# Performance work log

Hardware: AMD Instinct MI355X
Metric: run time of the kernel (lower is better)

Reference implementation:

```python
import jax, jax.numpy as jnp
import numpy as np

B = 16384
F_CONT = 128   # continuous features (Gaussian scopes)
F_CAT = 128    # integer-valued features (Categorical scopes)
NG = 1024      # number of Gaussian leaves
NC = 1024      # number of Categorical leaves
K = 32         # categorical classes
LOG_2PI = float(np.log(2.0 * np.pi))


def setup_inputs() -> dict:
    key = jax.random.key(0)
    k1, k2, k3, k4, k5, k6, k7 = jax.random.split(key, 7)
    # data: first F_CONT columns continuous, last F_CAT columns hold integer category values
    x_cont = jax.random.normal(k1, (B, F_CONT), dtype=jnp.float32)
    x_cat = jax.random.randint(k2, (B, F_CAT), 0, K).astype(jnp.float32)
    x = jnp.concatenate([x_cont, x_cat], axis=1)  # [B, 256]
    gauss_mean = jax.random.normal(k3, (NG,), dtype=jnp.float32)
    gauss_std = jax.random.uniform(k4, (NG,), dtype=jnp.float32, minval=0.5, maxval=2.0)
    cat_logp = jax.nn.log_softmax(jax.random.normal(k5, (NC, K), dtype=jnp.float32), axis=-1)
    gauss_scopes = jax.random.randint(k6, (NG,), 0, F_CONT)            # index into continuous cols
    cat_scopes = jax.random.randint(k7, (NC,), 0, F_CAT) + F_CONT      # index into categorical cols
    return {
        "x": x,
        "gauss_mean": gauss_mean,
        "gauss_std": gauss_std,
        "cat_logp": cat_logp,
        "gauss_scopes": gauss_scopes,
        "cat_scopes": cat_scopes,
    }


def reference(x, gauss_mean, gauss_std, cat_logp, gauss_scopes, cat_scopes):
    # Fused equivalent of the per-leaf Python loop: one gather + one formula per family.
    # Gaussian leaves: Normal(mean, std).log_prob(x[:, scope])
    gv = x[:, gauss_scopes]                                   # [B, NG]
    z = (gv - gauss_mean[None, :]) / gauss_std[None, :]
    g_ll = -0.5 * (z * z) - jnp.log(gauss_std)[None, :] - 0.5 * LOG_2PI
    # Categorical leaves: log p_i[x[:, scope_i]]
    cidx = x[:, cat_scopes].astype(jnp.int32)                 # [B, NC]
    c_ll = cat_logp[jnp.arange(cat_logp.shape[0])[None, :], cidx]  # [B, NC]
    return jnp.concatenate([g_ll, c_ll], axis=1)              # [B, NG+NC]
```

## Files before the change

kernel.cpp:

```cpp
#include <hip/hip_runtime.h>
#include <math.h>


#define HALF_LOG_2PI 0.91893853320467274178f

constexpr int BROWS   = 16384;
constexpr int FX      = 256;
constexpr int NG      = 1024;
constexpr int NC      = 1024;
constexpr int KCAT    = 32;
constexpr int OUTW    = NG + NC;
constexpr int ROWS_PB = 16;
constexpr int NTHR    = 256;
constexpr int XPITCH  = FX + 1;
constexpr int CCH     = 128;
constexpr int NCHUNK  = NC / CCH;
constexpr int CPITCH  = CCH + 4;

__global__ __launch_bounds__(NTHR) void leaves_kernel(
    const float* __restrict__ x,
    const float* __restrict__ gmean,
    const float* __restrict__ gstd,
    const float* __restrict__ clogp,
    const int*   __restrict__ gsc,
    const int*   __restrict__ csc,
    float*       __restrict__ out)
{
    __shared__ float xs[ROWS_PB * XPITCH];
    __shared__ float cts[ROWS_PB * CPITCH];

    const int t = threadIdx.x;
    const long long b0 = (long long)blockIdx.x * ROWS_PB;

    {
        const int r  = t >> 4;
        const int c0 = (t & 15) * 16;
        const float* src = x + (b0 + r) * FX + c0;
        float*       dst = xs + r * XPITCH + c0;
        #pragma unroll
        for (int q = 0; q < 4; ++q) {
            float4 v = ((const float4*)src)[q];
            dst[q * 4 + 0] = v.x; dst[q * 4 + 1] = v.y;
            dst[q * 4 + 2] = v.z; dst[q * 4 + 3] = v.w;
        }
    }

    const int4   g4 = ((const int4*)gsc)[t];
    const float4 mu = ((const float4*)gmean)[t];
    const float4 sd = ((const float4*)gstd)[t];
    float4 is, cc;
    is.x = 1.0f / sd.x;  cc.x = -logf(sd.x) - HALF_LOG_2PI;
    is.y = 1.0f / sd.y;  cc.y = -logf(sd.y) - HALF_LOG_2PI;
    is.z = 1.0f / sd.z;  cc.z = -logf(sd.z) - HALF_LOG_2PI;
    is.w = 1.0f / sd.w;  cc.w = -logf(sd.w) - HALF_LOG_2PI;

    __syncthreads();

    #pragma unroll
    for (int r = 0; r < ROWS_PB; ++r) {
        const float* xr = xs + r * XPITCH;
        float4 gres;
        { float z = (xr[g4.x] - mu.x) * is.x; gres.x = fmaf(-0.5f * z, z, cc.x); }
        { float z = (xr[g4.y] - mu.y) * is.y; gres.y = fmaf(-0.5f * z, z, cc.y); }
        { float z = (xr[g4.z] - mu.z) * is.z; gres.z = fmaf(-0.5f * z, z, cc.z); }
        { float z = (xr[g4.w] - mu.w) * is.w; gres.w = fmaf(-0.5f * z, z, cc.w); }
        ((float4*)(out + (b0 + r) * OUTW))[t] = gres;
    }

    const int w   = t >> 6;
    const int l   = t & 63;
    const int row = l & 15;
    const int co  = l >> 4;
    const float* xrp = xs + row * XPITCH;

    const int wr = t >> 4;
    const int wo = (t & 15) * 4;

    for (int chunk = 0; chunk < NCHUNK; ++chunk) {
        const int cb = chunk * CCH + w * 32 + co;

        int sc[8];
        #pragma unroll
        for (int j = 0; j < 8; ++j) sc[j] = csc[cb + j * 4];

        int ix[8];
        #pragma unroll
        for (int j = 0; j < 8; ++j) ix[j] = (int)xrp[sc[j]];

        float v[8];
        #pragma unroll
        for (int j = 0; j < 8; ++j) v[j] = clogp[(cb + j * 4) * KCAT + ix[j]];

        #pragma unroll
        for (int j = 0; j < 8; ++j)
            cts[row * CPITCH + w * 32 + j * 4 + co] = v[j];

        __syncthreads();

        {
            float4 a = *(const float4*)(cts + wr * CPITCH + wo);
            float4 b = *(const float4*)(cts + wr * CPITCH + wo + 64);
            float* dst = out + (b0 + wr) * OUTW + NG + chunk * CCH;
            *(float4*)(dst + wo)      = a;
            *(float4*)(dst + wo + 64) = b;
        }
        __syncthreads();
    }
}

extern "C" void kernel_launch(void* const* d_in, const int* in_sizes, int n_in,
                              void* d_out, int out_size, void* d_ws, size_t ws_size,
                              hipStream_t stream) {
    const float* x     = (const float*)d_in[0];
    const float* gmean = (const float*)d_in[1];
    const float* gstd  = (const float*)d_in[2];
    const float* clogp = (const float*)d_in[3];
    const int*   gsc   = (const int*)d_in[4];
    const int*   csc   = (const int*)d_in[5];
    float*       out   = (float*)d_out;

    leaves_kernel<<<dim3(BROWS / ROWS_PB), dim3(NTHR), 0, stream>>>(
        x, gmean, gstd, clogp, gsc, csc, out);
}
```

Measured before the change: 30.53 us.

## Double-buffer categorical staging tile and prefetch first chunk before Gaussian pass

The categorical staging buffer in shared memory is split into two halves. Each chunk's gathers now overlap with writing out the previous chunk, which removes one of the two barriers per chunk. The first chunk's dependent gathers (scope, x value, log-prob) are issued before the Gaussian output loop, so their latency hides behind the Gaussian stores. This costs extra shared memory and keeps eight values live across the Gaussian loop, which raises register pressure.

```diff
diff --git a/kernel.cpp b/kernel.cpp
--- a/kernel.cpp
+++ b/kernel.cpp
@@ -27,7 +27,7 @@
     float*       __restrict__ out)
 {
     __shared__ float xs[ROWS_PB * XPITCH];
-    __shared__ float cts[ROWS_PB * CPITCH];
+    __shared__ float cts[2][ROWS_PB * CPITCH];
 
     const int t = threadIdx.x;
     const long long b0 = (long long)blockIdx.x * ROWS_PB;
@@ -56,6 +56,25 @@
 
     __syncthreads();
 
+    const int w   = t >> 6;
+    const int l   = t & 63;
+    const int row = l & 15;
+    const int co  = l >> 4;
+    const float* xrp = xs + row * XPITCH;
+
+    const int wr = t >> 4;
+    const int wo = (t & 15) * 4;
+
+    float v[8];
+    {
+        const int cb = 0 * CCH + w * 32 + co;
+        #pragma unroll
+        for (int j = 0; j < 8; ++j) {
+            const int c = cb + j * 4;
+            v[j] = clogp[c * KCAT + (int)xrp[csc[c]]];
+        }
+    }
+
     #pragma unroll
     for (int r = 0; r < ROWS_PB; ++r) {
         const float* xr = xs + r * XPITCH;
@@ -67,44 +86,44 @@
         ((float4*)(out + (b0 + r) * OUTW))[t] = gres;
     }
 
-    const int w   = t >> 6;
-    const int l   = t & 63;
-    const int row = l & 15;
-    const int co  = l >> 4;
-    const float* xrp = xs + row * XPITCH;
+    #pragma unroll
+    for (int j = 0; j < 8; ++j)
+        cts[0][row * CPITCH + w * 32 + j * 4 + co] = v[j];
+    __syncthreads();
 
-    const int wr = t >> 4;
-    const int wo = (t & 15) * 4;
-
-    for (int chunk = 0; chunk < NCHUNK; ++chunk) {
+    for (int chunk = 1; chunk < NCHUNK; ++chunk) {
+        const int p  = chunk & 1;
         const int cb = chunk * CCH + w * 32 + co;
 
-        int sc[8];
         #pragma unroll
-        for (int j = 0; j < 8; ++j) sc[j] = csc[cb + j * 4];
+        for (int j = 0; j < 8; ++j) {
+            const int c = cb + j * 4;
+            v[j] = clogp[c * KCAT + (int)xrp[csc[c]]];
+        }
 
-        int ix[8];
-        #pragma unroll
-        for (int j = 0; j < 8; ++j) ix[j] = (int)xrp[sc[j]];
-
-        float v[8];
-        #pragma unroll
-        for (int j = 0; j < 8; ++j) v[j] = clogp[(cb + j * 4) * KCAT + ix[j]];
+        {
+            const float* src = cts[p ^ 1] + wr * CPITCH;
+            float4 a = *(const float4*)(src + wo);
+            float4 b = *(const float4*)(src + wo + 64);
+            float* dst = out + (b0 + wr) * OUTW + NG + (chunk - 1) * CCH;
+            *(float4*)(dst + wo)      = a;
+            *(float4*)(dst + wo + 64) = b;
+        }
 
         #pragma unroll
         for (int j = 0; j < 8; ++j)
-            cts[row * CPITCH + w * 32 + j * 4 + co] = v[j];
+            cts[p][row * CPITCH + w * 32 + j * 4 + co] = v[j];
 
         __syncthreads();
+    }
 
-        {
-            float4 a = *(const float4*)(cts + wr * CPITCH + wo);
-            float4 b = *(const float4*)(cts + wr * CPITCH + wo + 64);
-            float* dst = out + (b0 + wr) * OUTW + NG + chunk * CCH;
-            *(float4*)(dst + wo)      = a;
-            *(float4*)(dst + wo + 64) = b;
-        }
-        __syncthreads();
+    {
+        const float* src = cts[(NCHUNK - 1) & 1] + wr * CPITCH;
+        float4 a = *(const float4*)(src + wo);
+        float4 b = *(const float4*)(src + wo + 64);
+        float* dst = out + (b0 + wr) * OUTW + NG + (NCHUNK - 1) * CCH;
+        *(float4*)(dst + wo)      = a;
+        *(float4*)(dst + wo + 64) = b;
     }
 }
 
```

New measurement: 31.34 us. 1.03x slower.
